# Kernel tuning notes

Hardware: AMD Instinct MI355X
Metric: run time of the kernel (lower is better)

## Reference

```python
import jax, jax.numpy as jnp
import numpy as np

NUM_HEADS = 8


def setup_inputs() -> dict:
    key = jax.random.key(0)
    k1, k2, k3, k4, k5 = jax.random.split(key, 5)
    N, L, D = 256, 512, 256
    x = jax.random.normal(k1, (N, L, D), dtype=jnp.float32)
    dist_bias = jax.random.normal(k2, (N, N), dtype=jnp.float32)
    w_qkv = jax.random.normal(k3, (3 * D, D), dtype=jnp.float32) * (D ** -0.5)
    w_proj = jax.random.normal(k4, (D, D), dtype=jnp.float32) * (D ** -0.5)
    b_proj = jax.random.normal(k5, (D,), dtype=jnp.float32) * 0.02
    return {"x": x, "dist_bias": dist_bias, "w_qkv": w_qkv,
            "w_proj": w_proj, "b_proj": b_proj}


def reference(x, dist_bias, w_qkv, w_proj, b_proj):
    # x: (N, L, D)  attention over the SAMPLE axis N, per (head, position)
    N, L, D = x.shape
    H = NUM_HEADS
    hd = D // H
    scale = hd ** -0.5

    qkv = jnp.einsum('nld,ed->nle', x, w_qkv)              # (N, L, 3D)
    qkv = qkv.reshape(N, L, 3, H, hd)
    q = jnp.transpose(qkv[:, :, 0], (2, 1, 0, 3))          # (H, L, N, hd)
    k = jnp.transpose(qkv[:, :, 1], (2, 1, 0, 3))
    v = jnp.transpose(qkv[:, :, 2], (2, 1, 0, 3))

    # scores over sample axis, with additive genetic-distance bias
    scores = jnp.einsum('hlnd,hlmd->hlnm', q, k) * scale   # (H, L, N, N)
    scores = scores + dist_bias[None, None, :, :]
    attn = jax.nn.softmax(scores, axis=-1)                 # dropout p=0.0

    out = jnp.einsum('hlnm,hlmd->hlnd', attn, v)           # (H, L, N, hd)
    out = jnp.transpose(out, (2, 1, 0, 3)).reshape(N, L, D)
    return jnp.einsum('nld,ed->nle', out, w_proj) + b_proj
```

## Files before the change

### kernel.cpp

```cpp
#include <hip/hip_runtime.h>
#include <stdint.h>

#define NS 256
#define LS 512
#define DS 256
#define HS 8
#define HD 32
#define SCALE 0.17677669529663687f
#define LOG2E 1.4426950408889634f
#define QSCALE (SCALE * LOG2E)

typedef __attribute__((ext_vector_type(4))) float f32x4;
typedef __attribute__((ext_vector_type(8))) __bf16 bf16x8;
typedef __attribute__((ext_vector_type(4))) __bf16 bf16x4;
typedef __attribute__((ext_vector_type(8))) unsigned short ushort8;

static __device__ __forceinline__ unsigned short f2bf(float f) {
  unsigned int u = __builtin_bit_cast(unsigned int, f);
  u += 0x7fffu + ((u >> 16) & 1u);
  return (unsigned short)(u >> 16);
}

static __device__ __forceinline__ void gld16(const void* g, void* l) {
  __builtin_amdgcn_global_load_lds((const __attribute__((address_space(1))) void*)g,
                                   (__attribute__((address_space(3))) void*)l, 16, 0, 0);
}

static __device__ __forceinline__ f32x4 mfma16(bf16x8 a, bf16x8 b, f32x4 c) {
  return __builtin_amdgcn_mfma_f32_16x16x32_bf16(a, b, c, 0, 0, 0);
}

__global__ void k_cvt(const float* __restrict__ in, unsigned short* __restrict__ out, int n) {
  int stride = gridDim.x * blockDim.x;
  for (int i = blockIdx.x * blockDim.x + threadIdx.x; i * 8 < n; i += stride) {
    int b = i * 8;
    float4 a0 = *(const float4*)(in + b);
    float4 a1 = *(const float4*)(in + b + 4);
    ushort8 o;
    o[0] = f2bf(a0.x); o[1] = f2bf(a0.y); o[2] = f2bf(a0.z); o[3] = f2bf(a0.w);
    o[4] = f2bf(a1.x); o[5] = f2bf(a1.y); o[6] = f2bf(a1.z); o[7] = f2bf(a1.w);
    *(ushort8*)(out + b) = o;
  }
}

__global__ __launch_bounds__(256) void k_qkv(const unsigned short* __restrict__ xb,
                                             const unsigned short* __restrict__ wq,
                                             unsigned short* __restrict__ qkv) {
  __shared__ unsigned short As[128 * 64];
  __shared__ unsigned short Bs[128 * 64];
  const int tid = threadIdx.x, lane = tid & 63, wid = tid >> 6;
  const int bid = blockIdx.x;
  const int et = bid % 6, rt = bid / 6;
  const int l = rt >> 1, n0 = (rt & 1) << 7;
  const int wr = wid >> 1, wc = wid & 1;

  f32x4 acc[4][4] = {};
  const int rowA = lane >> 3;
  const int kkA = (lane & 7) * 8;

  for (int kt = 0; kt < 4; ++kt) {
    __syncthreads();
    const int k0 = kt * 64;
    for (int p = 0; p < 4; ++p) {
      const int chunk = p * 4 + wid;
      const int row = chunk * 8 + rowA;
      const unsigned short* gA = xb + (((size_t)(n0 + row)) * LS + l) * DS + k0 + kkA;
      gld16(gA, &As[chunk * 8 * 64]);
      const unsigned short* gB = wq + ((size_t)(et * 128 + row)) * DS + k0 + kkA;
      gld16(gB, &Bs[chunk * 8 * 64]);
    }
    __syncthreads();
    for (int kf = 0; kf < 2; ++kf) {
      const int ko = kf * 32 + (lane >> 4) * 8;
      bf16x8 a[4], b[4];
      for (int m = 0; m < 4; ++m)
        a[m] = *(const bf16x8*)&As[(wr * 64 + m * 16 + (lane & 15)) * 64 + ko];
      for (int nn = 0; nn < 4; ++nn)
        b[nn] = *(const bf16x8*)&Bs[(wc * 64 + nn * 16 + (lane & 15)) * 64 + ko];
      for (int m = 0; m < 4; ++m)
        for (int nn = 0; nn < 4; ++nn)
          acc[m][nn] = mfma16(a[m], b[nn], acc[m][nn]);
    }
  }

  const int rbase = (lane >> 4) * 4, cbase = lane & 15;
  for (int m = 0; m < 4; ++m)
    for (int nn = 0; nn < 4; ++nn) {
      const int e = et * 128 + wc * 64 + nn * 16 + cbase;
      const int which = e >> 8, h = (e >> 5) & 7, d = e & 31;
      const float qs = (which == 0) ? QSCALE : 1.0f;
      const size_t base = (((size_t)which * HS + h) * LS + l) * (NS * HD) + d;
      for (int j = 0; j < 4; ++j) {
        const int n = n0 + wr * 64 + m * 16 + rbase + j;
        qkv[base + (size_t)n * HD] = f2bf(acc[m][nn][j] * qs);
      }
    }
}

__global__ __launch_bounds__(256, 4) void k_attn(const unsigned short* __restrict__ qkv,
                                                 const float* __restrict__ dist,
                                                 unsigned short* __restrict__ att) {
  __shared__ unsigned short Vt[32][NS + 8];
  __shared__ __bf16 Pl[4][16][68];
  const int tid = threadIdx.x, lane = tid & 63, wid = tid >> 6;
  const int bid = blockIdx.x;
  const int h = bid >> 10, l = (bid >> 1) & 511, half = bid & 1;
  const int n0 = half << 7;
  const unsigned short* qb = qkv + (((size_t)0 * HS + h) * LS + l) * (NS * HD);
  const unsigned short* kb = qkv + (((size_t)1 * HS + h) * LS + l) * (NS * HD);
  const unsigned short* vb = qkv + (((size_t)2 * HS + h) * LS + l) * (NS * HD);

  {
    const unsigned short* vr = vb + tid * HD;
    for (int c = 0; c < 4; ++c) {
      ushort8 v8 = *(const ushort8*)(vr + c * 8);
      for (int jj = 0; jj < 8; ++jj) Vt[c * 8 + jj][tid] = v8[jj];
    }
  }

  const int fr = lane & 15, g = lane >> 4, fk = g * 8;
  const int wq0 = n0 + wid * 32;
  bf16x8 qf[2];
#pragma unroll
  for (int m = 0; m < 2; ++m)
    qf[m] = *(const bf16x8*)(qb + (size_t)(wq0 + m * 16 + fr) * HD + fk);

  f32x4 o[2][2] = {};
  float mo[2] = {-1e30f, -1e30f}, ls[2] = {0.f, 0.f};

  __syncthreads();

  for (int cb = 0; cb < 4; ++cb) {
    const int c0 = cb * 64;
    bf16x8 kfr[4];
#pragma unroll
    for (int nn = 0; nn < 4; ++nn)
      kfr[nn] = *(const bf16x8*)(kb + (size_t)(c0 + nn * 16 + fr) * HD + fk);

#pragma unroll
    for (int m = 0; m < 2; ++m) {
      const int qg = wq0 + m * 16 + fr;
      float4 bv[4];
#pragma unroll
      for (int nn = 0; nn < 4; ++nn)
        bv[nn] = *(const float4*)(dist + (size_t)qg * NS + c0 + nn * 16 + g * 4);

      f32x4 z = {};
      f32x4 s[4];
#pragma unroll
      for (int nn = 0; nn < 4; ++nn) s[nn] = mfma16(kfr[nn], qf[m], z);

      float mx = -1e30f;
#pragma unroll
      for (int nn = 0; nn < 4; ++nn) {
#pragma unroll
        for (int j = 0; j < 4; ++j) {
          const float b = (j == 0) ? bv[nn].x : (j == 1) ? bv[nn].y
                        : (j == 2) ? bv[nn].z : bv[nn].w;
          const float v = fmaf(b, LOG2E, s[nn][j]);
          s[nn][j] = v;
          mx = fmaxf(mx, v);
        }
      }
      mx = fmaxf(mx, __shfl_xor(mx, 16));
      mx = fmaxf(mx, __shfl_xor(mx, 32));
      const float mn = fmaxf(mo[m], mx);
      const float fsc = __builtin_exp2f(mo[m] - mn);
      mo[m] = mn;

      float rs = 0.f;
#pragma unroll
      for (int nn = 0; nn < 4; ++nn) {
        bf16x4 pk;
#pragma unroll
        for (int j = 0; j < 4; ++j) {
          const float p = __builtin_exp2f(s[nn][j] - mn);
          rs += p;
          pk[j] = (__bf16)p;
        }
        *(bf16x4*)&Pl[wid][fr][nn * 16 + g * 4] = pk;
      }
      rs += __shfl_xor(rs, 16);
      rs += __shfl_xor(rs, 32);
      ls[m] = ls[m] * fsc + rs;

#pragma unroll
      for (int j = 0; j < 4; ++j) {
        const float fo = __shfl(fsc, g * 4 + j);
        o[m][0][j] *= fo;
        o[m][1][j] *= fo;
      }

#pragma unroll
      for (int kf = 0; kf < 2; ++kf) {
        const int ko = kf * 32 + fk;
        bf16x8 pa = *(const bf16x8*)&Pl[wid][fr][ko];
#pragma unroll
        for (int df = 0; df < 2; ++df) {
          bf16x8 vv = *(const bf16x8*)&Vt[df * 16 + fr][c0 + ko];
          o[m][df] = mfma16(pa, vv, o[m][df]);
        }
      }
    }
  }

#pragma unroll
  for (int m = 0; m < 2; ++m) {
    const float inv = 1.0f / ls[m];
#pragma unroll
    for (int j = 0; j < 4; ++j) {
      const float invo = __shfl(inv, g * 4 + j);
      const int n = wq0 + m * 16 + g * 4 + j;
      const size_t ob = ((size_t)n * LS + l) * DS + h * HD;
      att[ob + 0 * 16 + fr] = f2bf(o[m][0][j] * invo);
      att[ob + 1 * 16 + fr] = f2bf(o[m][1][j] * invo);
    }
  }
}

__global__ __launch_bounds__(256) void k_proj(const unsigned short* __restrict__ ab,
                                              const unsigned short* __restrict__ wp,
                                              const float* __restrict__ bp,
                                              float* __restrict__ out) {
  __shared__ unsigned short As[128 * 64];
  __shared__ unsigned short Bs[128 * 64];
  const int tid = threadIdx.x, lane = tid & 63, wid = tid >> 6;
  const int bid = blockIdx.x;
  const int et = bid & 1, rt = bid >> 1;
  const int wr = wid >> 1, wc = wid & 1;

  f32x4 acc[4][4] = {};
  const int rowA = lane >> 3;
  const int kkA = (lane & 7) * 8;

  for (int kt = 0; kt < 4; ++kt) {
    __syncthreads();
    const int k0 = kt * 64;
    for (int p = 0; p < 4; ++p) {
      const int chunk = p * 4 + wid;
      const int row = chunk * 8 + rowA;
      const unsigned short* gA = ab + ((size_t)(rt * 128 + row)) * DS + k0 + kkA;
      gld16(gA, &As[chunk * 8 * 64]);
      const unsigned short* gB = wp + ((size_t)(et * 128 + row)) * DS + k0 + kkA;
      gld16(gB, &Bs[chunk * 8 * 64]);
    }
    __syncthreads();
    for (int kf = 0; kf < 2; ++kf) {
      const int ko = kf * 32 + (lane >> 4) * 8;
      bf16x8 a[4], b[4];
      for (int m = 0; m < 4; ++m)
        a[m] = *(const bf16x8*)&As[(wr * 64 + m * 16 + (lane & 15)) * 64 + ko];
      for (int nn = 0; nn < 4; ++nn)
        b[nn] = *(const bf16x8*)&Bs[(wc * 64 + nn * 16 + (lane & 15)) * 64 + ko];
      for (int m = 0; m < 4; ++m)
        for (int nn = 0; nn < 4; ++nn)
          acc[m][nn] = mfma16(a[m], b[nn], acc[m][nn]);
    }
  }

  const int rbase = (lane >> 4) * 4, cbase = lane & 15;
  for (int m = 0; m < 4; ++m)
    for (int nn = 0; nn < 4; ++nn) {
      const int e = et * 128 + wc * 64 + nn * 16 + cbase;
      const float bv = bp[e];
      for (int j = 0; j < 4; ++j) {
        const size_t mm = (size_t)rt * 128 + wr * 64 + m * 16 + rbase + j;
        out[mm * DS + e] = acc[m][nn][j] + bv;
      }
    }
}

extern "C" void kernel_launch(void* const* d_in, const int* in_sizes, int n_in,
                              void* d_out, int out_size, void* d_ws, size_t ws_size,
                              hipStream_t stream) {
  const float* x     = (const float*)d_in[0];
  const float* dist  = (const float*)d_in[1];
  const float* wqkv  = (const float*)d_in[2];
  const float* wproj = (const float*)d_in[3];
  const float* bproj = (const float*)d_in[4];
  float* out = (float*)d_out;

  unsigned short* ws   = (unsigned short*)d_ws;
  unsigned short* xb   = ws;
  unsigned short* wqb  = xb + 33554432;
  unsigned short* wpb  = wqb + 196608;
  unsigned short* qkvb = wpb + 65536;
  unsigned short* attb = qkvb + 100663296;

  k_cvt<<<8192, 256, 0, stream>>>(x, xb, 33554432);
  k_cvt<<<96, 256, 0, stream>>>(wqkv, wqb, 196608);
  k_cvt<<<32, 256, 0, stream>>>(wproj, wpb, 65536);
  k_qkv<<<6144, 256, 0, stream>>>(xb, wqb, qkvb);
  k_attn<<<8192, 256, 0, stream>>>(qkvb, dist, attb);
  k_proj<<<2048, 256, 0, stream>>>(attb, wpb, bproj, out);
}
```

Baseline: 562.6 us.

## Replace online softmax with two-pass full-row softmax in attention kernel

The attention kernel now computes all 256 scores per query row into registers first, takes a single row max, then does the exponentials and the PV products. This removes the online-softmax rescaling: no per-chunk exp of the old max, no shuffles to rescale the accumulators, no running-sum update. The distance bias is also folded into the MFMA accumulator input instead of a separate FMA pass. The cost is higher register pressure from holding 64 score values per lane, so the occupancy hint is lowered from 4 to 3 blocks, which may reduce latency hiding.

```diff
diff --git a/kernel.cpp b/kernel.cpp
--- a/kernel.cpp
+++ b/kernel.cpp
@@ -97,7 +97,7 @@
     }
 }
 
-__global__ __launch_bounds__(256, 4) void k_attn(const unsigned short* __restrict__ qkv,
+__global__ __launch_bounds__(256, 3) void k_attn(const unsigned short* __restrict__ qkv,
                                                  const float* __restrict__ dist,
                                                  unsigned short* __restrict__ att) {
   __shared__ unsigned short Vt[32][NS + 8];
@@ -125,95 +125,83 @@
   for (int m = 0; m < 2; ++m)
     qf[m] = *(const bf16x8*)(qb + (size_t)(wq0 + m * 16 + fr) * HD + fk);
 
-  f32x4 o[2][2] = {};
-  float mo[2] = {-1e30f, -1e30f}, ls[2] = {0.f, 0.f};
-
   __syncthreads();
 
-  for (int cb = 0; cb < 4; ++cb) {
-    const int c0 = cb * 64;
-    bf16x8 kfr[4];
-#pragma unroll
-    for (int nn = 0; nn < 4; ++nn)
-      kfr[nn] = *(const bf16x8*)(kb + (size_t)(c0 + nn * 16 + fr) * HD + fk);
-
-#pragma unroll
-    for (int m = 0; m < 2; ++m) {
-      const int qg = wq0 + m * 16 + fr;
-      float4 bv[4];
+#pragma unroll
+  for (int m = 0; m < 2; ++m) {
+    const int qg = wq0 + m * 16 + fr;
+    f32x4 s[4][4];
+
+#pragma unroll
+    for (int cb = 0; cb < 4; ++cb) {
+      const int c0 = cb * 64;
+      bf16x8 kfr[4];
 #pragma unroll
       for (int nn = 0; nn < 4; ++nn)
-        bv[nn] = *(const float4*)(dist + (size_t)qg * NS + c0 + nn * 16 + g * 4);
-
-      f32x4 z = {};
-      f32x4 s[4];
-#pragma unroll
-      for (int nn = 0; nn < 4; ++nn) s[nn] = mfma16(kfr[nn], qf[m], z);
-
-      float mx = -1e30f;
+        kfr[nn] = *(const bf16x8*)(kb + (size_t)(c0 + nn * 16 + fr) * HD + fk);
 #pragma unroll
       for (int nn = 0; nn < 4; ++nn) {
-#pragma unroll
-        for (int j = 0; j < 4; ++j) {
-          const float b = (j == 0) ? bv[nn].x : (j == 1) ? bv[nn].y
-                        : (j == 2) ? bv[nn].z : bv[nn].w;
-          const float v = fmaf(b, LOG2E, s[nn][j]);
-          s[nn][j] = v;
-          mx = fmaxf(mx, v);
-        }
-      }
-      mx = fmaxf(mx, __shfl_xor(mx, 16));
-      mx = fmaxf(mx, __shfl_xor(mx, 32));
-      const float mn = fmaxf(mo[m], mx);
-      const float fsc = __builtin_exp2f(mo[m] - mn);
-      mo[m] = mn;
-
-      float rs = 0.f;
+        const float4 bvv = *(const float4*)(dist + (size_t)qg * NS + c0 + nn * 16 + g * 4);
+        f32x4 c;
+        c[0] = bvv.x * LOG2E; c[1] = bvv.y * LOG2E;
+        c[2] = bvv.z * LOG2E; c[3] = bvv.w * LOG2E;
+        s[cb][nn] = mfma16(kfr[nn], qf[m], c);
+      }
+    }
+
+    float vmax[4];
+#pragma unroll
+    for (int cb = 0; cb < 4; ++cb) {
+      float a0 = fmaxf(fmaxf(s[cb][0][0], s[cb][0][1]), fmaxf(s[cb][0][2], s[cb][0][3]));
+      float a1 = fmaxf(fmaxf(s[cb][1][0], s[cb][1][1]), fmaxf(s[cb][1][2], s[cb][1][3]));
+      float a2 = fmaxf(fmaxf(s[cb][2][0], s[cb][2][1]), fmaxf(s[cb][2][2], s[cb][2][3]));
+      float a3 = fmaxf(fmaxf(s[cb][3][0], s[cb][3][1]), fmaxf(s[cb][3][2], s[cb][3][3]));
+      vmax[cb] = fmaxf(fmaxf(a0, a1), fmaxf(a2, a3));
+    }
+    float mx = fmaxf(fmaxf(vmax[0], vmax[1]), fmaxf(vmax[2], vmax[3]));
+    mx = fmaxf(mx, __shfl_xor(mx, 16));
+    mx = fmaxf(mx, __shfl_xor(mx, 32));
+
+    f32x4 o0 = {}, o1 = {};
+    float rcb[4];
+#pragma unroll
+    for (int cb = 0; cb < 4; ++cb) {
+      const int c0 = cb * 64;
+      float r = 0.f;
 #pragma unroll
       for (int nn = 0; nn < 4; ++nn) {
         bf16x4 pk;
 #pragma unroll
         for (int j = 0; j < 4; ++j) {
-          const float p = __builtin_exp2f(s[nn][j] - mn);
-          rs += p;
+          const float p = __builtin_exp2f(s[cb][nn][j] - mx);
+          r += p;
           pk[j] = (__bf16)p;
         }
         *(bf16x4*)&Pl[wid][fr][nn * 16 + g * 4] = pk;
       }
-      rs += __shfl_xor(rs, 16);
-      rs += __shfl_xor(rs, 32);
-      ls[m] = ls[m] * fsc + rs;
-
-#pragma unroll
-      for (int j = 0; j < 4; ++j) {
-        const float fo = __shfl(fsc, g * 4 + j);
-        o[m][0][j] *= fo;
-        o[m][1][j] *= fo;
-      }
-
+      rcb[cb] = r;
 #pragma unroll
       for (int kf = 0; kf < 2; ++kf) {
         const int ko = kf * 32 + fk;
         bf16x8 pa = *(const bf16x8*)&Pl[wid][fr][ko];
-#pragma unroll
-        for (int df = 0; df < 2; ++df) {
-          bf16x8 vv = *(const bf16x8*)&Vt[df * 16 + fr][c0 + ko];
-          o[m][df] = mfma16(pa, vv, o[m][df]);
-        }
-      }
-    }
-  }
-
-#pragma unroll
-  for (int m = 0; m < 2; ++m) {
-    const float inv = 1.0f / ls[m];
+        bf16x8 vv0 = *(const bf16x8*)&Vt[fr][c0 + ko];
+        bf16x8 vv1 = *(const bf16x8*)&Vt[16 + fr][c0 + ko];
+        o0 = mfma16(pa, vv0, o0);
+        o1 = mfma16(pa, vv1, o1);
+      }
+    }
+    float rs = (rcb[0] + rcb[1]) + (rcb[2] + rcb[3]);
+    rs += __shfl_xor(rs, 16);
+    rs += __shfl_xor(rs, 32);
+    const float inv = 1.0f / rs;
+
 #pragma unroll
     for (int j = 0; j < 4; ++j) {
       const float invo = __shfl(inv, g * 4 + j);
       const int n = wq0 + m * 16 + g * 4 + j;
       const size_t ob = ((size_t)n * LS + l) * DS + h * HD;
-      att[ob + 0 * 16 + fr] = f2bf(o[m][0][j] * invo);
-      att[ob + 1 * 16 + fr] = f2bf(o[m][1][j] * invo);
+      att[ob + fr]      = f2bf(o0[j] * invo);
+      att[ob + 16 + fr] = f2bf(o1[j] * invo);
     }
   }
 }
```

New measurement: 608.9 us. 1.08x slower.
